# Optimization experiments

Hardware: AMD Instinct MI355X
Metric: run time of the kernel (lower is better)

## Reference

```python
import jax, jax.numpy as jnp
import numpy as np

B = 256
PERIOD = 256
F = B * PERIOD            # total frames
N1 = F * 6                # encoder nodes (6 arm joints per frame)
E1 = F * 5
N2 = F * 14               # decoder nodes (14 robot joints per frame)
E2 = F * 13


def spatial_block(x, ei, ea, Wl, bl, Wu, bu):
    # PyG flow source_to_target: x_i = x[ei[1]] (target), x_j = x[ei[0]] (source)
    z = jnp.concatenate([x[ei[1]], x[ei[0]], ea], axis=-1)
    m = jax.nn.leaky_relu(z @ Wl.T + bl, 0.01)          # torch default negative_slope
    agg = jax.ops.segment_sum(m, ei[1], num_segments=x.shape[0])  # aggr='add'
    return agg + x @ Wu.T + bu                           # residual upsample(x)


def temporal_block(x, ei, Wl, bl):
    z = jnp.concatenate([x[ei[1]], x[ei[0]]], axis=-1)
    m = jax.nn.relu(z @ Wl.T + bl)
    s = jax.ops.segment_sum(m, ei[1], num_segments=x.shape[0])
    cnt = jax.ops.segment_sum(jnp.ones((ei.shape[1],), x.dtype), ei[1], num_segments=x.shape[0])
    return s / jnp.maximum(cnt, 1.0)[:, None] + x        # aggr='mean' + residual


def forward(x, edge_index, edge_attr, temporal_edge_index, lower, upper,
            edge_index2, edge_attr2, temporal_edge_index2,
            We1_l, be1_l, We1_u, be1_u, We2_l, be2_l, We2_u, be2_u,
            We3_l, be3_l, We3_u, be3_u, Wt1, bt1, W_tr, b_tr,
            Wd1_l, bd1_l, Wd1_u, bd1_u, Wd2_l, bd2_l, Wd2_u, bd2_u,
            Wd3_l, bd3_l, Wd3_u, bd3_u, Wt2, bt2):
    # Encoder: 6 -> 16 -> 32 -> 64 spatial, then temporal
    h = spatial_block(x, edge_index, edge_attr, We1_l, be1_l, We1_u, be1_u)
    h = spatial_block(h, edge_index, edge_attr, We2_l, be2_l, We2_u, be2_u)
    h = spatial_block(h, edge_index, edge_attr, We3_l, be3_l, We3_u, be3_u)
    z = temporal_block(h, temporal_edge_index, Wt1, bt1)
    # transform: [N1,64] -> [B*PERIOD, 6*64] -> Linear(384,896) -> tanh -> [N2,64]
    z = jnp.tanh(z.reshape(B * PERIOD, 6 * 64) @ W_tr.T + b_tr).reshape(-1, 64)
    # Decoder: concat(z, lower, upper) -> 66 -> 32 -> 16 -> 1, temporal, tanh
    x2 = jnp.concatenate([z, lower, upper], axis=1)
    h = spatial_block(x2, edge_index2, edge_attr2, Wd1_l, bd1_l, Wd1_u, bd1_u)
    h = spatial_block(h, edge_index2, edge_attr2, Wd2_l, bd2_l, Wd2_u, bd2_u)
    h = spatial_block(h, edge_index2, edge_attr2, Wd3_l, bd3_l, Wd3_u, bd3_u)
    out = jnp.tanh(temporal_block(h, temporal_edge_index2, Wt2, bt2))
    ang = lower + (upper - lower) * (out + 1.0) / 2.0
    return ang


def setup_inputs() -> dict:
    key = jax.random.key(0)
    ks = jax.random.split(key, 40)
    p = lambda i, shape: jax.random.normal(ks[i], shape, jnp.float32) * 0.1
    lower = jax.random.normal(ks[4], (N2, 1), jnp.float32)
    upper = lower + jax.random.uniform(ks[5], (N2, 1), jnp.float32)
    return {
        'x': jax.random.normal(ks[0], (N1, 6), jnp.float32),
        'edge_index': jax.random.randint(ks[1], (2, E1), 0, N1),
        'edge_attr': jax.random.normal(ks[2], (E1, 3), jnp.float32),
        'temporal_edge_index': jax.random.randint(ks[3], (2, N1), 0, N1),
        'lower': lower, 'upper': upper,
        'edge_index2': jax.random.randint(ks[6], (2, E2), 0, N2),
        'edge_attr2': jax.random.normal(ks[7], (E2, 6), jnp.float32),
        'temporal_edge_index2': jax.random.randint(ks[8], (2, N2), 0, N2),
        'We1_l': p(10, (16, 15)), 'be1_l': p(11, (16,)), 'We1_u': p(12, (16, 6)), 'be1_u': p(13, (16,)),
        'We2_l': p(14, (32, 35)), 'be2_l': p(15, (32,)), 'We2_u': p(16, (32, 16)), 'be2_u': p(17, (32,)),
        'We3_l': p(18, (64, 67)), 'be3_l': p(19, (64,)), 'We3_u': p(20, (64, 32)), 'be3_u': p(21, (64,)),
        'Wt1': p(22, (64, 128)), 'bt1': p(23, (64,)),
        'W_tr': p(24, (14 * 64, 6 * 64)), 'b_tr': p(25, (14 * 64,)),
        'Wd1_l': p(26, (32, 138)), 'bd1_l': p(27, (32,)), 'Wd1_u': p(28, (32, 66)), 'bd1_u': p(29, (32,)),
        'Wd2_l': p(30, (16, 70)), 'bd2_l': p(31, (16,)), 'Wd2_u': p(32, (16, 32)), 'bd2_u': p(33, (16,)),
        'Wd3_l': p(34, (1, 38)), 'bd3_l': p(35, (1,)), 'Wd3_u': p(36, (1, 16)), 'bd3_u': p(37, (1,)),
        'Wt2': p(38, (1, 2)), 'bt2': p(39, (1,)),
    }


def reference(x, edge_index, edge_attr, temporal_edge_index, lower, upper,
              edge_index2, edge_attr2, temporal_edge_index2,
              We1_l, be1_l, We1_u, be1_u, We2_l, be2_l, We2_u, be2_u,
              We3_l, be3_l, We3_u, be3_u, Wt1, bt1, W_tr, b_tr,
              Wd1_l, bd1_l, Wd1_u, bd1_u, Wd2_l, bd2_l, Wd2_u, bd2_u,
              Wd3_l, bd3_l, Wd3_u, bd3_u, Wt2, bt2):
    return forward(x, edge_index, edge_attr, temporal_edge_index, lower, upper,
                   edge_index2, edge_attr2, temporal_edge_index2,
                   We1_l, be1_l, We1_u, be1_u, We2_l, be2_l, We2_u, be2_u,
                   We3_l, be3_l, We3_u, be3_u, Wt1, bt1, W_tr, b_tr,
                   Wd1_l, bd1_l, Wd1_u, bd1_u, Wd2_l, bd2_l, Wd2_u, bd2_u,
                   Wd3_l, bd3_l, Wd3_u, bd3_u, Wt2, bt2)
```

## Files before the change

### kernel.cpp

```cpp
#include <hip/hip_runtime.h>
#include <hip/hip_bf16.h>


constexpr int kN1 = 393216;
constexpr int kE1 = 327680;
constexpr int kN2 = 917504;
constexpr int kE2 = 851968;
constexpr int kM  = 65536;
constexpr int kK  = 384;
constexpr int kN  = 896;

typedef __attribute__((ext_vector_type(8))) short bf16x8;
typedef __attribute__((ext_vector_type(4))) float f32x4;

__device__ inline float2 bf2_unpack(unsigned u) {
    union { unsigned i; float f; } a, b;
    a.i = u << 16;
    b.i = u & 0xffff0000u;
    return make_float2(a.f, b.f);
}

__device__ inline ushort f2bf(float f) {
    union { float f; unsigned u; } x; x.f = f;
    unsigned r = x.u + 0x7fffu + ((x.u >> 16) & 1u);
    return (ushort)(r >> 16);
}

__device__ inline void pack8(ushort* d, float4 u, float4 v) {
    bf16x8 p;
    p[0] = (short)f2bf(u.x); p[1] = (short)f2bf(u.y);
    p[2] = (short)f2bf(u.z); p[3] = (short)f2bf(u.w);
    p[4] = (short)f2bf(v.x); p[5] = (short)f2bf(v.y);
    p[6] = (short)f2bf(v.z); p[7] = (short)f2bf(v.w);
    *(bf16x8*)d = p;
}

template<int IN, int EA, int OUT, int TPB, int ITER>
__global__ __launch_bounds__(TPB)
void spatial_edge_kernel(const float* __restrict__ x,
                         const int* __restrict__ ei, int E,
                         const float* __restrict__ ea,
                         const float* __restrict__ Wl,
                         const float* __restrict__ bl,
                         float* __restrict__ out)
{
    constexpr int Z  = 2 * IN + EA;
    constexpr int Zp = (Z % 2 == 0) ? Z + 1 : Z;
    constexpr int EPB = TPB / OUT;
    static_assert(TPB % OUT == 0, "TPB % OUT");
    __shared__ float sW[OUT * Zp];
    __shared__ float sB[OUT];
    for (int i = threadIdx.x; i < OUT * Z; i += TPB)
        sW[(i / Z) * Zp + (i % Z)] = Wl[i];
    for (int i = threadIdx.x; i < OUT; i += TPB) sB[i] = bl[i];
    __syncthreads();

    const int le = threadIdx.x / OUT;
    const int c  = threadIdx.x % OUT;
    const float* __restrict__ w = &sW[c * Zp];
    const int base = blockIdx.x * EPB * ITER;

    #pragma unroll 1
    for (int it = 0; it < ITER; ++it) {
        const int e = base + it * EPB + le;
        if (e >= E) break;
        const int src = ei[e];
        const int dst = ei[E + e];
        float acc = sB[c];
        if constexpr (IN % 4 == 0) {
            const float4* __restrict__ xd4 = (const float4*)&x[(long)dst * IN];
            const float4* __restrict__ xs4 = (const float4*)&x[(long)src * IN];
            #pragma unroll
            for (int q = 0; q < IN / 4; ++q) {
                const float4 v = xd4[q];
                acc = fmaf(w[4*q+0], v.x, acc); acc = fmaf(w[4*q+1], v.y, acc);
                acc = fmaf(w[4*q+2], v.z, acc); acc = fmaf(w[4*q+3], v.w, acc);
            }
            #pragma unroll
            for (int q = 0; q < IN / 4; ++q) {
                const float4 v = xs4[q];
                acc = fmaf(w[IN+4*q+0], v.x, acc); acc = fmaf(w[IN+4*q+1], v.y, acc);
                acc = fmaf(w[IN+4*q+2], v.z, acc); acc = fmaf(w[IN+4*q+3], v.w, acc);
            }
        } else {
            const float* __restrict__ xd = &x[(long)dst * IN];
            const float* __restrict__ xs = &x[(long)src * IN];
            #pragma unroll
            for (int j = 0; j < IN; ++j) acc = fmaf(w[j], xd[j], acc);
            #pragma unroll
            for (int j = 0; j < IN; ++j) acc = fmaf(w[IN + j], xs[j], acc);
        }
        const float* __restrict__ eav = &ea[(long)e * EA];
        #pragma unroll
        for (int j = 0; j < EA; ++j) acc = fmaf(w[2 * IN + j], eav[j], acc);
        acc = acc > 0.f ? acc : 0.01f * acc;
        atomicAdd(&out[(long)dst * OUT + c], acc);
    }
}

template<int IN, int OUT, int ITER>
__global__ __launch_bounds__(256)
void upsample_kernel(const float* __restrict__ x, int N,
                     const float* __restrict__ Wu,
                     const float* __restrict__ bu,
                     float* __restrict__ out)
{
    constexpr int INp = (IN % 2 == 0) ? IN + 1 : IN;
    __shared__ float sW[OUT * INp];
    __shared__ float sB[OUT];
    for (int i = threadIdx.x; i < OUT * IN; i += 256)
        sW[(i / IN) * INp + (i % IN)] = Wu[i];
    for (int i = threadIdx.x; i < OUT; i += 256) sB[i] = bu[i];
    __syncthreads();

    const int total = N * OUT;
    #pragma unroll 1
    for (int it = 0; it < ITER; ++it) {
        const int idx = (blockIdx.x * ITER + it) * 256 + threadIdx.x;
        if (idx >= total) break;
        const int n = idx / OUT, c = idx % OUT;
        const float* __restrict__ w = &sW[c * INp];
        float acc = sB[c];
        if constexpr (IN % 4 == 0) {
            const float4* __restrict__ xv4 = (const float4*)&x[(long)n * IN];
            #pragma unroll
            for (int q = 0; q < IN / 4; ++q) {
                const float4 v = xv4[q];
                acc = fmaf(w[4*q+0], v.x, acc); acc = fmaf(w[4*q+1], v.y, acc);
                acc = fmaf(w[4*q+2], v.z, acc); acc = fmaf(w[4*q+3], v.w, acc);
            }
        } else {
            const float* __restrict__ xv = &x[(long)n * IN];
            #pragma unroll
            for (int j = 0; j < IN; ++j) acc = fmaf(w[j], xv[j], acc);
        }
        out[idx] = acc;
    }
}

template<int ITER>
__global__ __launch_bounds__(256)
void dec1_upsample_kernel(const __hip_bfloat16* __restrict__ zt,
                          const float* __restrict__ lo,
                          const float* __restrict__ up,
                          const float* __restrict__ Wu,
                          const float* __restrict__ bu,
                          float* __restrict__ out, int N)
{
    constexpr int IN = 66, INp = 67, OUT = 32;
    __shared__ float sW[OUT * INp];
    __shared__ float sB[OUT];
    for (int i = threadIdx.x; i < OUT * IN; i += 256)
        sW[(i / IN) * INp + (i % IN)] = Wu[i];
    if (threadIdx.x < OUT) sB[threadIdx.x] = bu[threadIdx.x];
    __syncthreads();

    const int total = N * OUT;
    #pragma unroll 1
    for (int it = 0; it < ITER; ++it) {
        const int idx = (blockIdx.x * ITER + it) * 256 + threadIdx.x;
        if (idx >= total) break;
        const int n = idx >> 5, c = idx & 31;
        const float* __restrict__ w = &sW[c * INp];
        const uint4* __restrict__ zn4 = (const uint4*)&zt[(long)n * 64];
        float acc = sB[c];
        #pragma unroll
        for (int q = 0; q < 8; ++q) {
            const uint4 u = zn4[q];
            float2 v;
            v = bf2_unpack(u.x); acc = fmaf(w[8*q+0], v.x, acc); acc = fmaf(w[8*q+1], v.y, acc);
            v = bf2_unpack(u.y); acc = fmaf(w[8*q+2], v.x, acc); acc = fmaf(w[8*q+3], v.y, acc);
            v = bf2_unpack(u.z); acc = fmaf(w[8*q+4], v.x, acc); acc = fmaf(w[8*q+5], v.y, acc);
            v = bf2_unpack(u.w); acc = fmaf(w[8*q+6], v.x, acc); acc = fmaf(w[8*q+7], v.y, acc);
        }
        acc = fmaf(w[64], lo[n], acc);
        acc = fmaf(w[65], up[n], acc);
        out[idx] = acc;
    }
}

__global__ __launch_bounds__(256)
void temporal_gemm_kernel(const float* __restrict__ x,
                          const int* __restrict__ ei, int E,
                          const float* __restrict__ Wt,
                          const float* __restrict__ bt,
                          float* __restrict__ s, float* __restrict__ cnt)
{
    constexpr int MT = 128, LDA = 136, LDB = 136;
    __shared__ ushort sA[MT * LDA];
    __shared__ ushort sB[64 * LDB];
    __shared__ float  sBias[64];
    __shared__ int    sDst[MT];

    const int tid = threadIdx.x;
    const int e0  = blockIdx.x * MT;

    for (int i = tid; i < 64 * 32; i += 256) {
        const int ch = i >> 5, q = i & 31;
        const float4 v = *(const float4*)&Wt[ch * 128 + q * 4];
        ushort* d = &sB[ch * LDB + q * 4];
        d[0] = f2bf(v.x); d[1] = f2bf(v.y); d[2] = f2bf(v.z); d[3] = f2bf(v.w);
    }
    if (tid < 64) sBias[tid] = bt[tid];

    {
        const int r  = tid >> 1, sh = tid & 1;
        const int e  = e0 + r;
        const int node = sh ? ei[e] : ei[E + e];
        const float4* __restrict__ xr = (const float4*)&x[(long)node * 64];
        ushort* d = &sA[r * LDA + sh * 64];
        #pragma unroll
        for (int q = 0; q < 16; q += 2)
            pack8(d + q * 4, xr[q], xr[q + 1]);
        if (sh == 0) {
            sDst[r] = node;
            atomicAdd(&cnt[node], 1.f);
        }
    }
    __syncthreads();

    const int lane = tid & 63, wid = tid >> 6;
    const int g = lane >> 4, rsel = lane & 15;
    f32x4 acc[2][4] = {};
    #pragma unroll
    for (int ks = 0; ks < 4; ++ks) {
        bf16x8 a_[2], b_[4];
        #pragma unroll
        for (int m = 0; m < 2; ++m)
            a_[m] = *(const bf16x8*)&sA[(wid*32 + m*16 + rsel) * LDA + ks*32 + g*8];
        #pragma unroll
        for (int n = 0; n < 4; ++n)
            b_[n] = *(const bf16x8*)&sB[(n*16 + rsel) * LDB + ks*32 + g*8];
        #pragma unroll
        for (int m = 0; m < 2; ++m)
            #pragma unroll
            for (int n = 0; n < 4; ++n)
                acc[m][n] = __builtin_amdgcn_mfma_f32_16x16x32_bf16(
                    a_[m], b_[n], acc[m][n], 0, 0, 0);
    }

    #pragma unroll
    for (int m = 0; m < 2; ++m) {
        #pragma unroll
        for (int rr = 0; rr < 4; ++rr) {
            const int row = wid*32 + m*16 + g*4 + rr;
            const long dst = sDst[row];
            #pragma unroll
            for (int n = 0; n < 4; ++n) {
                const int col = n*16 + rsel;
                const float v = fmaxf(acc[m][n][rr] + sBias[col], 0.f);
                atomicAdd(&s[dst * 64 + col], v);
            }
        }
    }
}

__global__ __launch_bounds__(256)
void dec1_gemm_kernel(const __hip_bfloat16* __restrict__ zt,
                      const float* __restrict__ lo, const float* __restrict__ up,
                      const int* __restrict__ ei, int E,
                      const float* __restrict__ ea,
                      const float* __restrict__ Wl,
                      const float* __restrict__ bl,
                      float* __restrict__ out)
{
    constexpr int MT = 128, LDA = 168, LDB = 168;
    __shared__ ushort sA[MT * LDA];
    __shared__ ushort sB[32 * LDB];
    __shared__ float  sBias[32];
    __shared__ int    sDst[MT];

    const int tid = threadIdx.x;
    const int e0  = blockIdx.x * MT;

    for (int i = tid; i < 32 * 160; i += 256) {
        const int ch = i / 160, j = i % 160;
        sB[ch * LDB + j] = (j < 138) ? f2bf(Wl[ch * 138 + j]) : (ushort)0;
    }
    if (tid < 32) sBias[tid] = bl[tid];

    {
        const int r  = tid >> 1, sh = tid & 1;
        const int e  = e0 + r;
        const int node = sh ? ei[e] : ei[E + e];
        ushort* d = &sA[r * LDA + sh * 66];
        uint* d32 = (uint*)d;
        const uint4* __restrict__ zr = (const uint4*)&zt[(long)node * 64];
        #pragma unroll
        for (int q = 0; q < 8; ++q) {
            const uint4 u = zr[q];
            d32[4*q+0] = u.x; d32[4*q+1] = u.y; d32[4*q+2] = u.z; d32[4*q+3] = u.w;
        }
        d[64] = f2bf(lo[node]);
        d[65] = f2bf(up[node]);
        if (sh) {
            const float* __restrict__ eav = &ea[(long)e * 6];
            #pragma unroll
            for (int j = 0; j < 6; ++j) d[66 + j] = f2bf(eav[j]);
            #pragma unroll
            for (int j = 72; j < 94; ++j) d[j] = 0;
        } else {
            sDst[r] = node;
        }
    }
    __syncthreads();

    const int lane = tid & 63, wid = tid >> 6;
    const int g = lane >> 4, rsel = lane & 15;
    f32x4 acc[2][2] = {};
    #pragma unroll
    for (int ks = 0; ks < 5; ++ks) {
        bf16x8 a_[2], b_[2];
        #pragma unroll
        for (int m = 0; m < 2; ++m)
            a_[m] = *(const bf16x8*)&sA[(wid*32 + m*16 + rsel) * LDA + ks*32 + g*8];
        #pragma unroll
        for (int n = 0; n < 2; ++n)
            b_[n] = *(const bf16x8*)&sB[(n*16 + rsel) * LDB + ks*32 + g*8];
        #pragma unroll
        for (int m = 0; m < 2; ++m)
            #pragma unroll
            for (int n = 0; n < 2; ++n)
                acc[m][n] = __builtin_amdgcn_mfma_f32_16x16x32_bf16(
                    a_[m], b_[n], acc[m][n], 0, 0, 0);
    }

    #pragma unroll
    for (int m = 0; m < 2; ++m) {
        #pragma unroll
        for (int rr = 0; rr < 4; ++rr) {
            const int row = wid*32 + m*16 + g*4 + rr;
            const long dst = sDst[row];
            #pragma unroll
            for (int n = 0; n < 2; ++n) {
                const int col = n*16 + rsel;
                float v = acc[m][n][rr] + sBias[col];
                v = v > 0.f ? v : 0.01f * v;
                atomicAdd(&out[dst * 32 + col], v);
            }
        }
    }
}

__global__ void temporal_combine64_kernel(const float* __restrict__ s,
                                          const float* __restrict__ cnt,
                                          const float* __restrict__ x,
                                          float* __restrict__ z, int N)
{
    int idx = blockIdx.x * blockDim.x + threadIdx.x;
    if (idx >= N * 64) return;
    const int n = idx >> 6;
    z[idx] = s[idx] / fmaxf(cnt[n], 1.f) + x[idx];
}

__global__ void temporal_edge1_kernel(const float* __restrict__ x,
                                      const int* __restrict__ ei, int E,
                                      const float* __restrict__ Wt,
                                      const float* __restrict__ bt,
                                      float* __restrict__ s, float* __restrict__ cnt)
{
    int e = blockIdx.x * blockDim.x + threadIdx.x;
    if (e >= E) return;
    const int src = ei[e];
    const int dst = ei[E + e];
    float m = Wt[0] * x[dst] + Wt[1] * x[src] + bt[0];
    m = fmaxf(m, 0.f);
    atomicAdd(&s[dst], m);
    atomicAdd(&cnt[dst], 1.f);
}

__global__ __launch_bounds__(256)
void gemm_mfma_tanh_kernel(const float* __restrict__ A,
                           const float* __restrict__ W,
                           const float* __restrict__ bias,
                           __hip_bfloat16* __restrict__ out)
{
    constexpr int BM = 128, LDP = 40;
    __shared__ ushort sA[BM * LDP];
    __shared__ ushort sB[BM * LDP];
    const int tid  = threadIdx.x;
    const int lane = tid & 63;
    const int wid  = tid >> 6;
    const int wr = wid >> 1, wc = wid & 1;
    const long bm = (long)blockIdx.y * BM;
    const long bn = (long)blockIdx.x * BM;

    const int sr = tid >> 1;
    const int sh = tid & 1;
    const float* __restrict__ gA = &A[(bm + sr) * kK + sh * 16];
    const float* __restrict__ gB = &W[(bn + sr) * kK + sh * 16];
    ushort* dA = &sA[sr * LDP + sh * 16];
    ushort* dB = &sB[sr * LDP + sh * 16];

    f32x4 acc[4][4] = {};
    const int g    = lane >> 4;
    const int rsel = lane & 15;

    for (int k0 = 0; k0 < kK; k0 += 32) {
        const float4 a0 = *(const float4*)(gA + k0 + 0);
        const float4 a1 = *(const float4*)(gA + k0 + 4);
        const float4 a2 = *(const float4*)(gA + k0 + 8);
        const float4 a3 = *(const float4*)(gA + k0 + 12);
        const float4 b0 = *(const float4*)(gB + k0 + 0);
        const float4 b1 = *(const float4*)(gB + k0 + 4);
        const float4 b2 = *(const float4*)(gB + k0 + 8);
        const float4 b3 = *(const float4*)(gB + k0 + 12);
        __syncthreads();
        pack8(dA, a0, a1); pack8(dA + 8, a2, a3);
        pack8(dB, b0, b1); pack8(dB + 8, b2, b3);
        __syncthreads();

        bf16x8 af[4], bfm[4];
        #pragma unroll
        for (int m = 0; m < 4; ++m)
            af[m] = *(const bf16x8*)&sA[(wr * 64 + m * 16 + rsel) * LDP + g * 8];
        #pragma unroll
        for (int n = 0; n < 4; ++n)
            bfm[n] = *(const bf16x8*)&sB[(wc * 64 + n * 16 + rsel) * LDP + g * 8];
        #pragma unroll
        for (int m = 0; m < 4; ++m)
            #pragma unroll
            for (int n = 0; n < 4; ++n)
                acc[m][n] = __builtin_amdgcn_mfma_f32_16x16x32_bf16(
                    af[m], bfm[n], acc[m][n], 0, 0, 0);
    }

    const long colb = bn + wc * 64 + (lane & 15);
    const long rowb = bm + wr * 64 + (lane >> 4) * 4;
    #pragma unroll
    for (int n = 0; n < 4; ++n) {
        const long col = colb + n * 16;
        const float bs = bias[col];
        #pragma unroll
        for (int m = 0; m < 4; ++m) {
            #pragma unroll
            for (int r = 0; r < 4; ++r) {
                const float v = tanhf(acc[m][n][r] + bs);
                out[(rowb + m * 16 + r) * kN + col] = __float2bfloat16(v);
            }
        }
    }
}

__global__ void final_kernel(const float* __restrict__ s,
                             const float* __restrict__ cnt,
                             const float* __restrict__ d3,
                             const float* __restrict__ lo,
                             const float* __restrict__ up,
                             float* __restrict__ out, int N)
{
    int i = blockIdx.x * blockDim.x + threadIdx.x;
    if (i >= N) return;
    const float t = s[i] / fmaxf(cnt[i], 1.f) + d3[i];
    const float o = tanhf(t);
    out[i] = lo[i] + (up[i] - lo[i]) * (o + 1.f) * 0.5f;
}

extern "C" void kernel_launch(void* const* d_in, const int* in_sizes, int n_in,
                              void* d_out, int out_size, void* d_ws, size_t ws_size,
                              hipStream_t stream)
{
    const float* x     = (const float*)d_in[0];
    const int*   ei1   = (const int*)  d_in[1];
    const float* ea1   = (const float*)d_in[2];
    const int*   tei1  = (const int*)  d_in[3];
    const float* lower = (const float*)d_in[4];
    const float* upper = (const float*)d_in[5];
    const int*   ei2   = (const int*)  d_in[6];
    const float* ea2   = (const float*)d_in[7];
    const int*   tei2  = (const int*)  d_in[8];
    const float* We1_l = (const float*)d_in[9];  const float* be1_l = (const float*)d_in[10];
    const float* We1_u = (const float*)d_in[11]; const float* be1_u = (const float*)d_in[12];
    const float* We2_l = (const float*)d_in[13]; const float* be2_l = (const float*)d_in[14];
    const float* We2_u = (const float*)d_in[15]; const float* be2_u = (const float*)d_in[16];
    const float* We3_l = (const float*)d_in[17]; const float* be3_l = (const float*)d_in[18];
    const float* We3_u = (const float*)d_in[19]; const float* be3_u = (const float*)d_in[20];
    const float* Wt1   = (const float*)d_in[21]; const float* bt1   = (const float*)d_in[22];
    const float* W_tr  = (const float*)d_in[23]; const float* b_tr  = (const float*)d_in[24];
    const float* Wd1_l = (const float*)d_in[25]; const float* bd1_l = (const float*)d_in[26];
    const float* Wd1_u = (const float*)d_in[27]; const float* bd1_u = (const float*)d_in[28];
    const float* Wd2_l = (const float*)d_in[29]; const float* bd2_l = (const float*)d_in[30];
    const float* Wd2_u = (const float*)d_in[31]; const float* bd2_u = (const float*)d_in[32];
    const float* Wd3_l = (const float*)d_in[33]; const float* bd3_l = (const float*)d_in[34];
    const float* Wd3_u = (const float*)d_in[35]; const float* bd3_u = (const float*)d_in[36];
    const float* Wt2   = (const float*)d_in[37]; const float* bt2   = (const float*)d_in[38];

    char* ws = (char*)d_ws;
    float* bufA = (float*)ws;
    float* bufB = (float*)(ws + 117440512);
    float* bufC = (float*)(ws + 234881024);
    __hip_bfloat16* zt = (__hip_bfloat16*)bufA;

    const int TPB = 256;
    auto cdiv = [](long a, long b) { return (int)((a + b - 1) / b); };

    upsample_kernel<6, 16, 8><<<cdiv((long)kN1 * 16, 2048), TPB, 0, stream>>>(
        x, kN1, We1_u, be1_u, bufA);
    spatial_edge_kernel<6, 3, 16, 256, 4><<<cdiv(kE1, 64), TPB, 0, stream>>>(
        x, ei1, kE1, ea1, We1_l, be1_l, bufA);

    upsample_kernel<16, 32, 8><<<cdiv((long)kN1 * 32, 2048), TPB, 0, stream>>>(
        bufA, kN1, We2_u, be2_u, bufB);
    spatial_edge_kernel<16, 3, 32, 256, 4><<<cdiv(kE1, 32), TPB, 0, stream>>>(
        bufA, ei1, kE1, ea1, We2_l, be2_l, bufB);

    upsample_kernel<32, 64, 8><<<cdiv((long)kN1 * 64, 2048), TPB, 0, stream>>>(
        bufB, kN1, We3_u, be3_u, bufA);
    spatial_edge_kernel<32, 3, 64, 256, 8><<<cdiv(kE1, 32), TPB, 0, stream>>>(
        bufB, ei1, kE1, ea1, We3_l, be3_l, bufA);

    hipMemsetAsync(bufB, 0, (size_t)kN1 * 64 * sizeof(float), stream);
    hipMemsetAsync(bufC, 0, (size_t)kN1 * sizeof(float), stream);
    temporal_gemm_kernel<<<kN1 / 128, 256, 0, stream>>>(
        bufA, tei1, kN1, Wt1, bt1, bufB, bufC);
    temporal_combine64_kernel<<<cdiv((long)kN1 * 64, TPB), TPB, 0, stream>>>(
        bufB, bufC, bufA, bufB, kN1);

    {
        dim3 grid(kN / 128, kM / 128);
        gemm_mfma_tanh_kernel<<<grid, 256, 0, stream>>>(bufB, W_tr, b_tr, zt);
    }

    dec1_upsample_kernel<8><<<cdiv((long)kN2 * 32, 2048), TPB, 0, stream>>>(
        zt, lower, upper, Wd1_u, bd1_u, bufB, kN2);
    dec1_gemm_kernel<<<kE2 / 128, 256, 0, stream>>>(
        zt, lower, upper, ei2, kE2, ea2, Wd1_l, bd1_l, bufB);

    float* d2 = (float*)bufA;
    upsample_kernel<32, 16, 8><<<cdiv((long)kN2 * 16, 2048), TPB, 0, stream>>>(
        bufB, kN2, Wd2_u, bd2_u, d2);
    spatial_edge_kernel<32, 6, 16, 256, 4><<<cdiv(kE2, 64), TPB, 0, stream>>>(
        bufB, ei2, kE2, ea2, Wd2_l, bd2_l, d2);

    float* d3 = bufB;
    upsample_kernel<16, 1, 8><<<cdiv(kN2, 2048), TPB, 0, stream>>>(
        d2, kN2, Wd3_u, bd3_u, d3);
    spatial_edge_kernel<16, 6, 1, 256, 1><<<cdiv(kE2, 256), TPB, 0, stream>>>(
        d2, ei2, kE2, ea2, Wd3_l, bd3_l, d3);

    hipMemsetAsync(bufC, 0, (size_t)2 * kN2 * sizeof(float), stream);
    temporal_edge1_kernel<<<cdiv(kN2, TPB), TPB, 0, stream>>>(
        d3, tei2, kN2, Wt2, bt2, bufC, bufC + kN2);
    final_kernel<<<cdiv(kN2, TPB), TPB, 0, stream>>>(
        bufC, bufC + kN2, d3, lower, upper, (float*)d_out, kN2);
}
```

Baseline: 1.568 ms.

## Use MFMA bf16 tile GEMM for spatial edge message layers

Adds a spatial_gemm_kernel that gathers 128 edges' concatenated target, source and edge-attribute features into shared memory as bf16. It computes the edge MLP with MFMA 16x16x32 instructions, then applies bias and leaky ReLU and scatters the results with atomicAdd. Three spatial edge layers (encoder 2 and 3, decoder 2) move from the scalar FMA per-channel kernel to this path, which is meant to cut redundant gathers and ALU work. The trade-off is bf16 rounding of activations and weights, plus K-padding waste.

```diff
diff --git a/kernel.cpp b/kernel.cpp
--- a/kernel.cpp
+++ b/kernel.cpp
@@ -95,6 +95,94 @@
         for (int j = 0; j < EA; ++j) acc = fmaf(w[2 * IN + j], eav[j], acc);
         acc = acc > 0.f ? acc : 0.01f * acc;
         atomicAdd(&out[(long)dst * OUT + c], acc);
+    }
+}
+
+template<int IN, int EA, int OUT, int KSTEPS>
+__global__ __launch_bounds__(256)
+void spatial_gemm_kernel(const float* __restrict__ x,
+                         const int* __restrict__ ei, int E,
+                         const float* __restrict__ ea,
+                         const float* __restrict__ Wl,
+                         const float* __restrict__ bl,
+                         float* __restrict__ out)
+{
+    constexpr int Z    = 2 * IN + EA;
+    constexpr int KPAD = KSTEPS * 32;
+    static_assert(Z <= KPAD, "K pad");
+    static_assert(IN % 8 == 0, "IN vec");
+    constexpr int LDA = KPAD + 8;
+    constexpr int MT  = 128;
+    constexpr int NF  = OUT / 16;
+    __shared__ ushort sA[MT * LDA];
+    __shared__ ushort sB[OUT * LDA];
+    __shared__ float  sBias[OUT];
+    __shared__ int    sDst[MT];
+
+    const int tid = threadIdx.x;
+    const int e0  = blockIdx.x * MT;
+
+    for (int i = tid; i < OUT * KPAD; i += 256) {
+        const int ch = i / KPAD, j = i % KPAD;
+        sB[ch * LDA + j] = (j < Z) ? f2bf(Wl[ch * Z + j]) : (ushort)0;
+    }
+    if (tid < OUT) sBias[tid] = bl[tid];
+
+    {
+        const int r  = tid >> 1, sh = tid & 1;
+        const int e  = e0 + r;
+        const int node = sh ? ei[e] : ei[E + e];
+        const float4* __restrict__ xr = (const float4*)&x[(long)node * IN];
+        ushort* d = &sA[r * LDA + sh * IN];
+        #pragma unroll
+        for (int q = 0; q < IN / 4; q += 2)
+            pack8(d + q * 4, xr[q], xr[q + 1]);
+        if (sh == 0) {
+            sDst[r] = node;
+        } else {
+            const float* __restrict__ eav = &ea[(long)e * EA];
+            #pragma unroll
+            for (int j = 0; j < EA; ++j) d[IN + j] = f2bf(eav[j]);
+            #pragma unroll
+            for (int j = Z; j < KPAD; ++j) sA[r * LDA + j] = 0;
+        }
+    }
+    __syncthreads();
+
+    const int lane = tid & 63, wid = tid >> 6;
+    const int g = lane >> 4, rsel = lane & 15;
+    f32x4 acc[2][NF] = {};
+    #pragma unroll
+    for (int ks = 0; ks < KSTEPS; ++ks) {
+        bf16x8 a_[2], b_[NF];
+        #pragma unroll
+        for (int m = 0; m < 2; ++m)
+            a_[m] = *(const bf16x8*)&sA[(wid*32 + m*16 + rsel) * LDA + ks*32 + g*8];
+        #pragma unroll
+        for (int n = 0; n < NF; ++n)
+            b_[n] = *(const bf16x8*)&sB[(n*16 + rsel) * LDA + ks*32 + g*8];
+        #pragma unroll
+        for (int m = 0; m < 2; ++m)
+            #pragma unroll
+            for (int n = 0; n < NF; ++n)
+                acc[m][n] = __builtin_amdgcn_mfma_f32_16x16x32_bf16(
+                    a_[m], b_[n], acc[m][n], 0, 0, 0);
+    }
+
+    #pragma unroll
+    for (int m = 0; m < 2; ++m) {
+        #pragma unroll
+        for (int rr = 0; rr < 4; ++rr) {
+            const int row = wid*32 + m*16 + g*4 + rr;
+            const long dst = sDst[row];
+            #pragma unroll
+            for (int n = 0; n < NF; ++n) {
+                const int col = n*16 + rsel;
+                float v = acc[m][n][rr] + sBias[col];
+                v = v > 0.f ? v : 0.01f * v;
+                atomicAdd(&out[dst * OUT + col], v);
+            }
+        }
     }
 }
 
@@ -501,12 +589,12 @@
 
     upsample_kernel<16, 32, 8><<<cdiv((long)kN1 * 32, 2048), TPB, 0, stream>>>(
         bufA, kN1, We2_u, be2_u, bufB);
-    spatial_edge_kernel<16, 3, 32, 256, 4><<<cdiv(kE1, 32), TPB, 0, stream>>>(
+    spatial_gemm_kernel<16, 3, 32, 2><<<kE1 / 128, TPB, 0, stream>>>(
         bufA, ei1, kE1, ea1, We2_l, be2_l, bufB);
 
     upsample_kernel<32, 64, 8><<<cdiv((long)kN1 * 64, 2048), TPB, 0, stream>>>(
         bufB, kN1, We3_u, be3_u, bufA);
-    spatial_edge_kernel<32, 3, 64, 256, 8><<<cdiv(kE1, 32), TPB, 0, stream>>>(
+    spatial_gemm_kernel<32, 3, 64, 3><<<kE1 / 128, TPB, 0, stream>>>(
         bufB, ei1, kE1, ea1, We3_l, be3_l, bufA);
 
     hipMemsetAsync(bufB, 0, (size_t)kN1 * 64 * sizeof(float), stream);
@@ -529,7 +617,7 @@
     float* d2 = (float*)bufA;
     upsample_kernel<32, 16, 8><<<cdiv((long)kN2 * 16, 2048), TPB, 0, stream>>>(
         bufB, kN2, Wd2_u, bd2_u, d2);
-    spatial_edge_kernel<32, 6, 16, 256, 4><<<cdiv(kE2, 64), TPB, 0, stream>>>(
+    spatial_gemm_kernel<32, 6, 16, 3><<<kE2 / 128, TPB, 0, stream>>>(
         bufB, ei2, kE2, ea2, Wd2_l, bd2_l, d2);
 
     float* d3 = bufB;
```

Measured after the change: 1.405 ms. 1.12x faster.
